# Kernel tuning notes

Hardware: AMD Instinct MI355X
Metric: run time of the kernel (lower is better)

## Reference

```python
import jax, jax.numpy as jnp
import numpy as np

N_NODES = 100000
N_EDGES = 1600000
N_GRAPHS = 1024
DIM_IN = 128
DIM_SELF = 16
BN_EPS = 1e-5


def _bn(x, gamma, beta):
    # training-mode BatchNorm1d over dim 0 (biased variance, as torch uses for normalization)
    m = jnp.mean(x, axis=0)
    v = jnp.mean((x - m) ** 2, axis=0)
    return gamma * (x - m) * jax.lax.rsqrt(v + BN_EPS) + beta


def _mlp(x, W1, b1, g, b, W2, b2):
    h = x @ W1 + b1
    h = jax.nn.relu(_bn(h, g, b))
    return h @ W2 + b2


def _gin(h, src, dst, W1, b1, g, b, W2, b2):
    # GINConv with eps=0: (1+eps)*h + sum over in-neighbors, then MLP
    agg = jax.ops.segment_sum(h[src], dst, num_segments=N_NODES)
    return _mlp(h + agg, W1, b1, g, b, W2, b2)


def setup_inputs() -> dict:
    key = jax.random.key(0)
    ks = jax.random.split(key, 16)

    def lin(k, fan_in, fan_out):
        bound = 1.0 / np.sqrt(fan_in)
        k1, k2 = jax.random.split(k)
        W = jax.random.uniform(k1, (fan_in, fan_out), jnp.float32, -bound, bound)
        b = jax.random.uniform(k2, (fan_out,), jnp.float32, -bound, bound)
        return W, b

    inp = {}
    inp['feat'] = jax.random.normal(ks[0], (N_NODES, DIM_IN), jnp.float32)
    inp['self_feat'] = jax.random.normal(ks[1], (N_GRAPHS, DIM_SELF), jnp.float32)
    inp['edge_src'] = jax.random.randint(ks[2], (N_EDGES,), 0, N_NODES, jnp.int32)
    inp['edge_dst'] = jax.random.randint(ks[3], (N_EDGES,), 0, N_NODES, jnp.int32)
    inp['node2graph'] = jnp.sort(jax.random.randint(ks[4], (N_NODES,), 0, N_GRAPHS, jnp.int32))

    inp['g1_W1'], inp['g1_b1'] = lin(ks[5], DIM_IN, 100)
    inp['g1_gamma'] = jnp.ones((100,), jnp.float32)
    inp['g1_beta'] = jnp.zeros((100,), jnp.float32)
    inp['g1_W2'], inp['g1_b2'] = lin(ks[6], 100, 100)

    inp['g2_W1'], inp['g2_b1'] = lin(ks[7], 100, 20)
    inp['g2_gamma'] = jnp.ones((20,), jnp.float32)
    inp['g2_beta'] = jnp.zeros((20,), jnp.float32)
    inp['g2_W2'], inp['g2_b2'] = lin(ks[8], 20, 20)

    inp['fc1_W'], inp['fc1_b'] = lin(ks[9], 20 * DIM_SELF, 32)
    inp['bn1_gamma'] = jnp.ones((32,), jnp.float32)
    inp['bn1_beta'] = jnp.zeros((32,), jnp.float32)
    inp['fc2_W'], inp['fc2_b'] = lin(ks[10], 32, 8)
    inp['bn2_gamma'] = jnp.ones((8,), jnp.float32)
    inp['bn2_beta'] = jnp.zeros((8,), jnp.float32)
    inp['fc3_W'], inp['fc3_b'] = lin(ks[11], 8, 1)
    return inp


def reference(feat, self_feat,
              g1_W1, g1_b1, g1_gamma, g1_beta, g1_W2, g1_b2,
              g2_W1, g2_b1, g2_gamma, g2_beta, g2_W2, g2_b2,
              fc1_W, fc1_b, bn1_gamma, bn1_beta,
              fc2_W, fc2_b, bn2_gamma, bn2_beta,
              fc3_W, fc3_b,
              edge_src, edge_dst, node2graph):
    h = _gin(feat, edge_src, edge_dst, g1_W1, g1_b1, g1_gamma, g1_beta, g1_W2, g1_b2)
    h = jax.nn.relu(h)
    h = _gin(h, edge_src, edge_dst, g2_W1, g2_b1, g2_gamma, g2_beta, g2_W2, g2_b2)
    h = jax.nn.relu(h)  # [N, 20]

    # dgl.mean_nodes: per-graph mean of node features
    sums = jax.ops.segment_sum(h, node2graph, num_segments=N_GRAPHS)  # [B, 20]
    cnts = jax.ops.segment_sum(jnp.ones((N_NODES,), h.dtype), node2graph, num_segments=N_GRAPHS)
    hg = sums / jnp.maximum(cnts, 1.0)[:, None]

    # kronecker fusion: bmm([B,20,1],[B,1,dim_self]) -> flatten
    kron = jnp.einsum('bi,bj->bij', hg, self_feat).reshape(N_GRAPHS, -1)  # [B, 20*dim_self]

    out = jax.nn.relu(_bn(kron @ fc1_W + fc1_b, bn1_gamma, bn1_beta))
    # dropout(0.3) is identity in eval mode
    out = jax.nn.relu(_bn(out @ fc2_W + fc2_b, bn2_gamma, bn2_beta))
    out = out @ fc3_W + fc3_b  # [B, dim_out]
    return out
```

## Files before the change

### kernel.cpp

```cpp
#include <hip/hip_runtime.h>

#define NN 100000
#define NE 1600000
#define NG 1024
#define DIN 128
#define D1 100
#define D2 20
#define DSELF 16
#define BN_EPS 1e-5f

#define NB 391
#define NBLK 782
#define EPB 2048
#define RAWCAP 5120
#define NAGG2 4000
#define NREP 64
#define APITCH 136

typedef unsigned int uint;
typedef unsigned short ushort;
typedef __attribute__((ext_vector_type(8))) short bfv8;
typedef __attribute__((ext_vector_type(4))) float fv4;

__device__ inline float bflo(uint x) { return __uint_as_float(x << 16); }
__device__ inline float bfhi(uint x) { return __uint_as_float(x & 0xffff0000u); }
__device__ inline uint packbf2(float a, float b) {
    uint ua = __float_as_uint(a), ub = __float_as_uint(b);
    ua += 0x7fffu + ((ua >> 16) & 1u);
    ub += 0x7fffu + ((ub >> 16) & 1u);
    return (ua >> 16) | (ub & 0xffff0000u);
}
__device__ inline ushort bfr(float x) {
    uint u = __float_as_uint(x);
    u += 0x7fffu + ((u >> 16) & 1u);
    return (ushort)(u >> 16);
}

__global__ __launch_bounds__(256) void k_gemm1(const float* __restrict__ feat,
                                               const float* __restrict__ W1,
                                               ushort* __restrict__ z1bf,
                                               float* __restrict__ pb1r) {
    __shared__ __align__(16) char smem[64 * APITCH * 2 + 112 * APITCH * 2];
    ushort* Al = (ushort*)smem;
    ushort* Bt = (ushort*)(smem + 64 * APITCH * 2);
    int t = threadIdx.x;
    if (blockIdx.x == 0) {
        for (int i = t; i < NREP * 200; i += 256) pb1r[i] = 0.f;
    }
    int row0 = blockIdx.x * 64;
#pragma unroll
    for (int i = 0; i < 8; i++) {
        int p = i * 256 + t;
        int r = p >> 5, cq = p & 31;
        int row = row0 + r; if (row >= NN) row = NN - 1;
        float4 v = *(const float4*)(feat + (size_t)row * DIN + cq * 4);
        ushort* dst = Al + r * APITCH + 4 * cq;
        dst[0] = bfr(v.x); dst[1] = bfr(v.y); dst[2] = bfr(v.z); dst[3] = bfr(v.w);
    }
    for (int p = t; p < 12800; p += 256) {
        int k = p / 100, n = p % 100;
        Bt[n * APITCH + k] = bfr(W1[p]);
    }
    __syncthreads();
    int w = __builtin_amdgcn_readfirstlane(t >> 6);
    int l = t & 63;
    int m16 = l & 15, quad = l >> 4;
    fv4 acc[7];
#pragma unroll
    for (int nt = 0; nt < 7; nt++) acc[nt] = (fv4){0.f, 0.f, 0.f, 0.f};
    const ushort* arow = Al + (w * 16 + m16) * APITCH;
#pragma unroll
    for (int kk = 0; kk < 4; kk++) {
        int kb = kk * 32 + quad * 8;
        bfv8 a = *(const bfv8*)(arow + kb);
#pragma unroll
        for (int nt = 0; nt < 7; nt++) {
            bfv8 b = *(const bfv8*)(Bt + (nt * 16 + m16) * APITCH + kb);
            acc[nt] = __builtin_amdgcn_mfma_f32_16x16x32_bf16(a, b, acc[nt], 0, 0, 0);
        }
    }
    __syncthreads();
    float* Ep = (float*)smem;
#pragma unroll
    for (int nt = 0; nt < 7; nt++) {
        int n = nt * 16 + m16;
        if (n < 100) {
#pragma unroll
            for (int rix = 0; rix < 4; rix++)
                Ep[(w * 16 + quad * 4 + rix) * 101 + n] = acc[nt][rix];
        }
    }
    __syncthreads();
#pragma unroll
    for (int i = 0; i < 13; i++) {
        int p = i * 256 + t;
        if (p < 3200) {
            int rr = p / 50, cc = 2 * (p % 50);
            int row = row0 + rr;
            if (row < NN) {
                float v0 = Ep[rr * 101 + cc], v1 = Ep[rr * 101 + cc + 1];
                *(uint*)(z1bf + (size_t)row * 100 + cc) = packbf2(v0, v1);
            }
        }
    }
}

__global__ __launch_bounds__(256) void k_csrA1(const int* __restrict__ dst,
                                               int* __restrict__ pbcount) {
    __shared__ int h[NB];
    int t = threadIdx.x, blk = blockIdx.x;
    for (int i = t; i < NB; i += 256) h[i] = 0;
    __syncthreads();
    int e0 = blk * EPB + t;
#pragma unroll
    for (int i = 0; i < 8; i++) {
        int e = e0 + i * 256;
        if (e < NE) atomicAdd(&h[dst[e] >> 8], 1);
    }
    __syncthreads();
    for (int i = t; i < NB; i += 256) pbcount[i * NBLK + blk] = h[i];
}

__global__ __launch_bounds__(1024) void k_csrS1(int* __restrict__ pbcount,
                                                int* __restrict__ btot) {
    __shared__ int s[1024];
    int t = threadIdx.x, b = blockIdx.x;
    int v = (t < NBLK) ? pbcount[b * NBLK + t] : 0;
    s[t] = v;
    __syncthreads();
    for (int off = 1; off < 1024; off <<= 1) {
        int x = (t >= off) ? s[t - off] : 0;
        __syncthreads();
        s[t] += x;
        __syncthreads();
    }
    if (t < NBLK) pbcount[b * NBLK + t] = s[t] - v;
    if (t == 1023) btot[b] = s[t];
}

__global__ __launch_bounds__(256) void k_csrA2(const int* __restrict__ src,
                                               const int* __restrict__ dst,
                                               const int* __restrict__ pbexcl,
                                               const int* __restrict__ btot,
                                               int* __restrict__ ebase_g,
                                               uint* __restrict__ gbuf) {
    __shared__ int cur[NB];
    __shared__ int sa[512], sb[512];
    int t = threadIdx.x, blk = blockIdx.x;
    int o0 = (t < NB) ? btot[t] : 0;
    int o1 = (t + 256 < NB) ? btot[t + 256] : 0;
    sa[t] = o0; sa[t + 256] = o1;
    __syncthreads();
    int* sp = sa; int* dp = sb;
    for (int off = 1; off < 512; off <<= 1) {
        dp[t] = sp[t] + ((t >= off) ? sp[t - off] : 0);
        int i2 = t + 256;
        dp[i2] = sp[i2] + ((i2 >= off) ? sp[i2 - off] : 0);
        __syncthreads();
        int* tmp = sp; sp = dp; dp = tmp;
    }
    if (t < NB)       cur[t]       = (sp[t] - o0) + pbexcl[t * NBLK + blk];
    if (t + 256 < NB) cur[t + 256] = (sp[t + 256] - o1) + pbexcl[(t + 256) * NBLK + blk];
    if (blk == 0) {
        if (t < NB)       ebase_g[t]       = sp[t] - o0;
        if (t + 256 < NB) ebase_g[t + 256] = sp[t + 256] - o1;
        if (t == 0)       ebase_g[NB]      = sp[NB - 1];
    }
    __syncthreads();
    int e0 = blk * EPB + t;
#pragma unroll
    for (int i = 0; i < 8; i++) {
        int e = e0 + i * 256;
        if (e < NE) {
            int d = dst[e];
            int b = d >> 8;
            int pos = atomicAdd(&cur[b], 1);
            gbuf[pos] = (uint)src[e] | ((uint)(d & 255) << 17);
        }
    }
}

__global__ __launch_bounds__(256) void k_csrB(const uint* __restrict__ gbuf,
                                              const int* __restrict__ ebase,
                                              int* __restrict__ deg,
                                              int* __restrict__ offs,
                                              int* __restrict__ srcS) {
    __shared__ uint raw[RAWCAP];
    __shared__ int srt[RAWCAP];
    __shared__ int pref[256], cur[256];
    int t = threadIdx.x, b = blockIdx.x;
    int e0 = ebase[b], e1 = ebase[b + 1];
    int cnt = e1 - e0; if (cnt > RAWCAP) cnt = RAWCAP;
    cur[t] = 0;
    for (int i = t; i < cnt; i += 256) raw[i] = gbuf[e0 + i];
    __syncthreads();
    for (int i = t; i < cnt; i += 256) atomicAdd(&cur[raw[i] >> 17], 1);
    __syncthreads();
    int v = cur[t];
    pref[t] = v;
    __syncthreads();
    for (int off = 1; off < 256; off <<= 1) {
        int x = (t >= off) ? pref[t - off] : 0;
        __syncthreads();
        pref[t] += x;
        __syncthreads();
    }
    int excl = pref[t] - v;
    int node = b * 256 + t;
    if (node < NN) { deg[node] = v; offs[node] = e0 + excl; }
    cur[t] = excl;
    __syncthreads();
    for (int i = t; i < cnt; i += 256) {
        uint p = raw[i];
        int lpos = atomicAdd(&cur[p >> 17], 1);
        srt[lpos] = (int)(p & 0x1FFFFu);
    }
    __syncthreads();
    for (int i = t; i < cnt; i += 256) srcS[e0 + i] = srt[i];
}

__global__ __launch_bounds__(1024) void k_agg1(const ushort* __restrict__ z1bf,
                                               const int* __restrict__ offs,
                                               const int* __restrict__ deg,
                                               const int* __restrict__ srcS,
                                               ushort* __restrict__ u1b,
                                               float* __restrict__ pb1r) {
    __shared__ float part[16][200];
    int t = threadIdx.x;
    int wq = __builtin_amdgcn_readfirstlane(t >> 6);
    int l = t & 63;
    int n = blockIdx.x * 16 + wq;
    int d = 0, base = 0;
    if (n < NN) { d = deg[n]; base = offs[n]; }
    bool act = (l < 50) && (n < NN);
    const ushort* zc = z1bf + 2 * l;
    float a0 = 0.f, a1 = 0.f, b0 = 0.f, b1 = 0.f;
    float c0 = 0.f, c1 = 0.f, e0 = 0.f, e1 = 0.f;
    int i = 0;
    for (; i + 8 <= d; i += 8) {
        int s0 = srcS[base + i],     s1 = srcS[base + i + 1];
        int s2 = srcS[base + i + 2], s3 = srcS[base + i + 3];
        int s4 = srcS[base + i + 4], s5 = srcS[base + i + 5];
        int s6 = srcS[base + i + 6], s7 = srcS[base + i + 7];
        if (act) {
            uint x0 = *(const uint*)(zc + (size_t)s0 * 100);
            uint x1 = *(const uint*)(zc + (size_t)s1 * 100);
            uint x2 = *(const uint*)(zc + (size_t)s2 * 100);
            uint x3 = *(const uint*)(zc + (size_t)s3 * 100);
            uint x4 = *(const uint*)(zc + (size_t)s4 * 100);
            uint x5 = *(const uint*)(zc + (size_t)s5 * 100);
            uint x6 = *(const uint*)(zc + (size_t)s6 * 100);
            uint x7 = *(const uint*)(zc + (size_t)s7 * 100);
            a0 += bflo(x0); a1 += bfhi(x0);
            b0 += bflo(x1); b1 += bfhi(x1);
            c0 += bflo(x2); c1 += bfhi(x2);
            e0 += bflo(x3); e1 += bfhi(x3);
            a0 += bflo(x4); a1 += bfhi(x4);
            b0 += bflo(x5); b1 += bfhi(x5);
            c0 += bflo(x6); c1 += bfhi(x6);
            e0 += bflo(x7); e1 += bfhi(x7);
        }
    }
    for (; i + 2 <= d; i += 2) {
        int s0 = srcS[base + i], s1 = srcS[base + i + 1];
        if (act) {
            uint x0 = *(const uint*)(zc + (size_t)s0 * 100);
            uint x1 = *(const uint*)(zc + (size_t)s1 * 100);
            a0 += bflo(x0); a1 += bfhi(x0);
            b0 += bflo(x1); b1 += bfhi(x1);
        }
    }
    if (i < d) {
        int s0 = srcS[base + i];
        if (act) {
            uint x0 = *(const uint*)(zc + (size_t)s0 * 100);
            a0 += bflo(x0); a1 += bfhi(x0);
        }
    }
    float r0 = 0.f, r1 = 0.f;
    if (act) {
        uint xs = *(const uint*)(zc + (size_t)n * 100);
        r0 = (a0 + b0) + (c0 + e0) + bflo(xs);
        r1 = (a1 + b1) + (c1 + e1) + bfhi(xs);
        *(uint*)(u1b + (size_t)n * 100 + 2 * l) = packbf2(r0, r1);
    }
    if (l < 50) {
        part[wq][2 * l] = r0;            part[wq][2 * l + 1] = r1;
        part[wq][100 + 2 * l] = r0 * r0; part[wq][100 + 2 * l + 1] = r1 * r1;
    }
    __syncthreads();
    if (t < 200) {
        float s = 0.f;
#pragma unroll
        for (int w2 = 0; w2 < 16; w2++) s += part[w2][t];
        atomicAdd(&pb1r[(blockIdx.x & (NREP - 1)) * 200 + t], s);
    }
}

__global__ __launch_bounds__(256) void k_bnfin100(const float* __restrict__ pb1r,
                                                  const float* __restrict__ gamma,
                                                  const float* __restrict__ beta,
                                                  float* __restrict__ sc,
                                                  float* __restrict__ sh) {
    __shared__ float red[200];
    int t = threadIdx.x;
    if (t < 200) {
        float s = 0.f;
#pragma unroll 8
        for (int r = 0; r < NREP; r++) s += pb1r[r * 200 + t];
        red[t] = s;
    }
    __syncthreads();
    if (t < 100) {
        float S = red[t], Q = red[100 + t];
        float mean = S * (1.f / NN);
        float var = Q * (1.f / NN) - mean * mean;
        float inv = rsqrtf(var + BN_EPS);
        float s = gamma[t] * inv;
        sc[t] = s;
        sh[t] = beta[t] - mean * s;
    }
}

__global__ __launch_bounds__(256) void k_m2(const ushort* __restrict__ u1b,
                                            const float* __restrict__ sc,
                                            const float* __restrict__ sh,
                                            const float* __restrict__ W2,
                                            const float* __restrict__ b2,
                                            const float* __restrict__ W1p,
                                            ushort* __restrict__ z2bf,
                                            float* __restrict__ pb2r) {
    __shared__ float Xs[100 * 65];
    int t = threadIdx.x;
    if (blockIdx.x == 0) {
        for (int i = t; i < NREP * 40; i += 256) pb2r[i] = 0.f;
    }
    int row0 = blockIdx.x * 64;
#pragma unroll
    for (int i = 0; i < 13; i++) {
        int p = i * 256 + t;
        if (p < 3200) {
            int r = p / 50, c = 2 * (p % 50);
            int row = row0 + r; if (row >= NN) row = NN - 1;
            uint x = *(const uint*)(u1b + (size_t)row * 100 + c);
            Xs[c * 65 + r] = fmaxf(bflo(x) * sc[c] + sh[c], 0.f);
            Xs[(c + 1) * 65 + r] = fmaxf(bfhi(x) * sc[c + 1] + sh[c + 1], 0.f);
        }
    }
    __syncthreads();
    int cg = __builtin_amdgcn_readfirstlane(t >> 6);
    int r = t & 63;
    int j0 = cg * 25;
    float H[25];
#pragma unroll
    for (int m = 0; m < 25; m++) H[m] = 0.f;
    for (int k = 0; k < D1; k++) {
        float a = Xs[k * 65 + r];
        const float* wr = W2 + k * D1 + j0;
#pragma unroll
        for (int m = 0; m < 25; m++) H[m] = fmaf(a, wr[m], H[m]);
    }
#pragma unroll
    for (int m = 0; m < 25; m++) H[m] = fmaxf(H[m] + b2[j0 + m], 0.f);
    float pz[20];
#pragma unroll
    for (int c = 0; c < 20; c++) pz[c] = 0.f;
#pragma unroll
    for (int m = 0; m < 25; m++) {
        const float* wp = W1p + (j0 + m) * D2;
#pragma unroll
        for (int c = 0; c < 20; c++) pz[c] = fmaf(H[m], wp[c], pz[c]);
    }
    __syncthreads();
    float* red = Xs;
#pragma unroll
    for (int c = 0; c < 20; c++) red[t * 20 + c] = pz[c];
    __syncthreads();
#pragma unroll
    for (int i = 0; i < 3; i++) {
        int p = i * 256 + t;
        if (p < 640) {
            int rr = p / 10, c2 = 2 * (p % 10);
            int row = row0 + rr;
            if (row < NN) {
                float v0 = red[rr * 20 + c2] + red[(64 + rr) * 20 + c2] +
                           red[(128 + rr) * 20 + c2] + red[(192 + rr) * 20 + c2];
                float v1 = red[rr * 20 + c2 + 1] + red[(64 + rr) * 20 + c2 + 1] +
                           red[(128 + rr) * 20 + c2 + 1] + red[(192 + rr) * 20 + c2 + 1];
                *(uint*)(z2bf + (size_t)row * 32 + c2) = packbf2(v0, v1);
            }
        }
    }
}

__global__ __launch_bounds__(256) void k_agg2(const ushort* __restrict__ z2bf,
                                              const int* __restrict__ offs,
                                              const int* __restrict__ deg,
                                              const int* __restrict__ srcS,
                                              float* __restrict__ u2,
                                              float* __restrict__ pb2r) {
    __shared__ float ls[500], lq[500];
    int t = threadIdx.x;
    int n = blockIdx.x * 25 + t / 10;
    int c2 = 2 * (t % 10);
    float r0 = 0.f, r1 = 0.f;
    if (t < 250 && n < NN) {
        int d = deg[n], base = offs[n];
        const ushort* zc = z2bf + c2;
        float a0 = 0.f, a1 = 0.f, b0 = 0.f, b1 = 0.f;
        int i = 0;
        for (; i + 2 <= d; i += 2) {
            uint x0 = *(const uint*)(zc + (size_t)srcS[base + i] * 32);
            uint x1 = *(const uint*)(zc + (size_t)srcS[base + i + 1] * 32);
            a0 += bflo(x0); a1 += bfhi(x0);
            b0 += bflo(x1); b1 += bfhi(x1);
        }
        if (i < d) {
            uint x0 = *(const uint*)(zc + (size_t)srcS[base + i] * 32);
            a0 += bflo(x0); a1 += bfhi(x0);
        }
        uint xs = *(const uint*)(zc + (size_t)n * 32);
        r0 = a0 + b0 + bflo(xs);
        r1 = a1 + b1 + bfhi(xs);
        *(float2*)(u2 + (size_t)n * D2 + c2) = make_float2(r0, r1);
    }
    if (t < 250) {
        int idx = (t / 10) * 20 + c2;
        ls[idx] = r0;     lq[idx] = r0 * r0;
        ls[idx + 1] = r1; lq[idx + 1] = r1 * r1;
    }
    __syncthreads();
    if (t < 20) {
        float S = 0.f, Q = 0.f;
#pragma unroll
        for (int j = 0; j < 25; j++) { S += ls[j * 20 + t]; Q += lq[j * 20 + t]; }
        int rep = (blockIdx.x & (NREP - 1)) * 40;
        atomicAdd(&pb2r[rep + t], S);
        atomicAdd(&pb2r[rep + 20 + t], Q);
    }
}

__global__ __launch_bounds__(64) void k_bnfin20(const float* __restrict__ pb2r,
                                                const float* __restrict__ gamma,
                                                const float* __restrict__ beta,
                                                float* __restrict__ sc,
                                                float* __restrict__ sh) {
    __shared__ float red[40];
    int t = threadIdx.x;
    if (t < 40) {
        float s = 0.f;
#pragma unroll 8
        for (int r = 0; r < NREP; r++) s += pb2r[r * 40 + t];
        red[t] = s;
    }
    __syncthreads();
    if (t < 20) {
        float S = red[t], Q = red[20 + t];
        float mean = S * (1.f / NN);
        float var = Q * (1.f / NN) - mean * mean;
        float inv = rsqrtf(var + BN_EPS);
        float s = gamma[t] * inv;
        sc[t] = s;
        sh[t] = beta[t] - mean * s;
    }
}

__global__ __launch_bounds__(256) void k_m3(const float* __restrict__ u2,
                                            const float* __restrict__ sc,
                                            const float* __restrict__ sh,
                                            const float* __restrict__ W2p,
                                            const float* __restrict__ b2p,
                                            float* __restrict__ h2) {
    int row = blockIdx.x * 256 + threadIdx.x;
    if (row >= NN) return;
    float ya[20];
    const float4* up = (const float4*)(u2 + (size_t)row * D2);
#pragma unroll
    for (int i = 0; i < 5; i++) {
        float4 v = up[i];
        float4 S = *(const float4*)(sc + 4 * i);
        float4 H = *(const float4*)(sh + 4 * i);
        ya[4 * i + 0] = fmaxf(v.x * S.x + H.x, 0.f);
        ya[4 * i + 1] = fmaxf(v.y * S.y + H.y, 0.f);
        ya[4 * i + 2] = fmaxf(v.z * S.z + H.z, 0.f);
        ya[4 * i + 3] = fmaxf(v.w * S.w + H.w, 0.f);
    }
    float hrow[D2];
#pragma unroll
    for (int j = 0; j < D2; j++) {
        float h = b2p[j];
#pragma unroll
        for (int k = 0; k < D2; k++) h = fmaf(ya[k], W2p[k * D2 + j], h);
        hrow[j] = fmaxf(h, 0.f);
    }
    float* hr = h2 + (size_t)row * D2;
#pragma unroll
    for (int c = 0; c < D2; c += 4) {
        float4 o; o.x = hrow[c]; o.y = hrow[c + 1]; o.z = hrow[c + 2]; o.w = hrow[c + 3];
        *(float4*)(hr + c) = o;
    }
}

__global__ __launch_bounds__(256) void k_pool(const float* __restrict__ h2,
                                              const int* __restrict__ n2g,
                                              float* __restrict__ hg) {
    int wq = __builtin_amdgcn_readfirstlane(threadIdx.x >> 6);
    int l = threadIdx.x & 63;
    int g = blockIdx.x * 4 + wq;
    if (g >= NG) return;
    int lo = 0, hi = NN;
    while (lo < hi) { int mid = (lo + hi) >> 1; if (n2g[mid] < g) lo = mid + 1; else hi = mid; }
    int s0 = lo;
    hi = NN;
    while (lo < hi) { int mid = (lo + hi) >> 1; if (n2g[mid] < g + 1) lo = mid + 1; else hi = mid; }
    int s1 = lo;
    float a = 0.f;
    if (l < 60) {
        int rg = l / 20, c = l % 20;
        for (int n = s0 + rg; n < s1; n += 3) a += h2[(size_t)n * D2 + c];
    }
    float v1 = __shfl(a, l + 20, 64);
    float v2 = __shfl(a, l + 40, 64);
    if (l < 20) {
        float cnt = (float)(s1 - s0);
        hg[g * D2 + l] = (a + v1 + v2) / fmaxf(cnt, 1.f);
    }
}

__global__ void k_head1(const float* __restrict__ hg, const float* __restrict__ sf,
                        const float* __restrict__ fc1W, float* __restrict__ a1) {
    int b = blockIdx.x * 8 + threadIdx.x / 32;
    int c = threadIdx.x % 32;
    if (b >= NG) return;
    const float* hgb = hg + b * D2;
    const float* sfb = sf + b * DSELF;
    float acc = 0.f;
    for (int i = 0; i < D2; i++) {
        float hi = hgb[i];
#pragma unroll
        for (int j = 0; j < DSELF; j++)
            acc += hi * sfb[j] * fc1W[(i * DSELF + j) * 32 + c];
    }
    a1[b * 32 + c] = acc;
}

__global__ __launch_bounds__(1024) void k_head2(
    const float* __restrict__ a1, const float* __restrict__ g1,
    const float* __restrict__ be1, const float* __restrict__ fc2W,
    const float* __restrict__ g2, const float* __restrict__ be2,
    const float* __restrict__ fc3W, const float* __restrict__ fc3b,
    float* __restrict__ out) {
    int t = threadIdx.x;
    int lane = t & 63, w = t >> 6;
    __shared__ float s1[16][32], s2[16][32];
    __shared__ float sc[32], sh[32], sc2[8], sh2[8];
    float x[32];
    const float4* ap = (const float4*)(a1 + t * 32);
#pragma unroll
    for (int i = 0; i < 8; i++) {
        float4 v = ap[i];
        x[4 * i] = v.x; x[4 * i + 1] = v.y; x[4 * i + 2] = v.z; x[4 * i + 3] = v.w;
    }
#pragma unroll
    for (int c = 0; c < 32; c++) {
        float v = x[c], q = v * v;
        for (int o = 32; o > 0; o >>= 1) {
            v += __shfl_down(v, o, 64);
            q += __shfl_down(q, o, 64);
        }
        if (lane == 0) { s1[w][c] = v; s2[w][c] = q; }
    }
    __syncthreads();
    if (t < 32) {
        float s = 0.f, q = 0.f;
        for (int ww = 0; ww < 16; ww++) { s += s1[ww][t]; q += s2[ww][t]; }
        float mean = s * (1.f / NG);
        float var = q * (1.f / NG) - mean * mean;
        float inv = rsqrtf(var + BN_EPS);
        float scl = g1[t] * inv;
        sc[t] = scl;
        sh[t] = be1[t] - mean * scl;
    }
    __syncthreads();
#pragma unroll
    for (int c = 0; c < 32; c++) x[c] = fmaxf(x[c] * sc[c] + sh[c], 0.f);
    float y[8];
#pragma unroll
    for (int p = 0; p < 8; p++) {
        float a = 0.f;
#pragma unroll
        for (int c = 0; c < 32; c++) a += x[c] * fc2W[c * 8 + p];
        y[p] = a;
    }
    __syncthreads();
#pragma unroll
    for (int p = 0; p < 8; p++) {
        float v = y[p], q = v * v;
        for (int o = 32; o > 0; o >>= 1) {
            v += __shfl_down(v, o, 64);
            q += __shfl_down(q, o, 64);
        }
        if (lane == 0) { s1[w][p] = v; s2[w][p] = q; }
    }
    __syncthreads();
    if (t < 8) {
        float s = 0.f, q = 0.f;
        for (int ww = 0; ww < 16; ww++) { s += s1[ww][t]; q += s2[ww][t]; }
        float mean = s * (1.f / NG);
        float var = q * (1.f / NG) - mean * mean;
        float inv = rsqrtf(var + BN_EPS);
        float scl = g2[t] * inv;
        sc2[t] = scl;
        sh2[t] = be2[t] - mean * scl;
    }
    __syncthreads();
    float o = fc3b[0];
#pragma unroll
    for (int p = 0; p < 8; p++) {
        float yy = fmaxf(y[p] * sc2[p] + sh2[p], 0.f);
        o += yy * fc3W[p];
    }
    out[t] = o;
}

extern "C" void kernel_launch(void* const* d_in, const int* in_sizes, int n_in,
                              void* d_out, int out_size, void* d_ws, size_t ws_size,
                              hipStream_t stream) {
    const float* feat    = (const float*)d_in[0];
    const float* sf      = (const float*)d_in[1];
    const int*   esrc    = (const int*)d_in[2];
    const int*   edst    = (const int*)d_in[3];
    const int*   n2g     = (const int*)d_in[4];
    const float* g1W1    = (const float*)d_in[5];
    const float* g1gam   = (const float*)d_in[7];
    const float* g1bet   = (const float*)d_in[8];
    const float* g1W2    = (const float*)d_in[9];
    const float* g1b2    = (const float*)d_in[10];
    const float* g2W1    = (const float*)d_in[11];
    const float* g2gam   = (const float*)d_in[13];
    const float* g2bet   = (const float*)d_in[14];
    const float* g2W2    = (const float*)d_in[15];
    const float* g2b2    = (const float*)d_in[16];
    const float* fc1W    = (const float*)d_in[17];
    const float* hbn1g   = (const float*)d_in[19];
    const float* hbn1b   = (const float*)d_in[20];
    const float* fc2W    = (const float*)d_in[21];
    const float* hbn2g   = (const float*)d_in[23];
    const float* hbn2b   = (const float*)d_in[24];
    const float* fc3W    = (const float*)d_in[25];
    const float* fc3b    = (const float*)d_in[26];
    float* out = (float*)d_out;

    char* w = (char*)d_ws;
    size_t off = 0;
    auto alloc = [&](size_t bytes) -> char* {
        char* p = w + off;
        off += (bytes + 15) & ~(size_t)15;
        return p;
    };
    char* regA = alloc((size_t)NN * 128 * 2);
    ushort* z1bf = (ushort*)regA;
    ushort* z2bf = (ushort*)regA;
    float*  u2   = (float*)(regA + 6400000);
    float*  h2   = (float*)(regA + 14400000);
    ushort* u1b  = (ushort*)alloc((size_t)NN * 100 * 2);
    int*   pbcnt = (int*)alloc((size_t)NB * NBLK * 4);
    int*   btot  = (int*)alloc(NB * 4);
    int*   ebase = (int*)alloc((NB + 1) * 4);
    uint*  gbuf  = (uint*)alloc((size_t)NE * 4);
    int*   deg   = (int*)alloc(NN * 4);
    int*   offs  = (int*)alloc(NN * 4);
    int*   srcS  = (int*)alloc((size_t)NE * 4);
    float* pb1r  = (float*)alloc((size_t)NREP * 200 * 4);
    float* pb2r  = (float*)alloc((size_t)NREP * 40 * 4);
    float* sc1   = (float*)alloc(D1 * 4);
    float* sh1   = (float*)alloc(D1 * 4);
    float* sc2   = (float*)alloc(D2 * 4);
    float* sh2   = (float*)alloc(D2 * 4);
    float* hg    = (float*)alloc(NG * D2 * 4);
    float* a1    = (float*)alloc(NG * 32 * 4);
    (void)in_sizes; (void)n_in; (void)out_size; (void)ws_size;

    k_gemm1<<<(NN + 63) / 64, 256, 0, stream>>>(feat, g1W1, z1bf, pb1r);

    k_csrA1<<<NBLK, 256, 0, stream>>>(edst, pbcnt);
    k_csrS1<<<NB, 1024, 0, stream>>>(pbcnt, btot);
    k_csrA2<<<NBLK, 256, 0, stream>>>(esrc, edst, pbcnt, btot, ebase, gbuf);
    k_csrB<<<NB, 256, 0, stream>>>(gbuf, ebase, deg, offs, srcS);

    k_agg1<<<NN / 16, 1024, 0, stream>>>(z1bf, offs, deg, srcS, u1b, pb1r);
    k_bnfin100<<<1, 256, 0, stream>>>(pb1r, g1gam, g1bet, sc1, sh1);
    k_m2<<<(NN + 63) / 64, 256, 0, stream>>>(u1b, sc1, sh1, g1W2, g1b2, g2W1, z2bf, pb2r);

    k_agg2<<<NAGG2, 256, 0, stream>>>(z2bf, offs, deg, srcS, u2, pb2r);
    k_bnfin20<<<1, 64, 0, stream>>>(pb2r, g2gam, g2bet, sc2, sh2);
    k_m3<<<(NN + 255) / 256, 256, 0, stream>>>(u2, sc2, sh2, g2W2, g2b2, h2);

    k_pool<<<(NG + 3) / 4, 256, 0, stream>>>(h2, n2g, hg);
    k_head1<<<NG / 8, 256, 0, stream>>>(hg, sf, fc1W, a1);
    k_head2<<<1, 1024, 0, stream>>>(a1, hbn1g, hbn1b, fc2W, hbn2g, hbn2b, fc3W, fc3b, out);
}
```

Baseline: 429.6 us.

## Pad z1 rows to 128 and process 16 nodes per wave in agg1

Pads the bf16 z1 gather buffer to a 128-element row pitch so that each gathered row starts on a 256-byte boundary. The agg1 kernel now uses 256-thread blocks where each wave walks 16 consecutive nodes. Each wave keeps its BatchNorm sum and sum-of-squares in registers and issues per-lane atomics once at the end, which removes the shared-memory reduction and the block-wide barrier. The cost is a larger z1 buffer and longer serial work per wave, which can leave waves unevenly loaded when node degrees differ.

```diff
diff --git a/kernel.cpp b/kernel.cpp
--- a/kernel.cpp
+++ b/kernel.cpp
@@ -99,7 +99,7 @@
             int row = row0 + rr;
             if (row < NN) {
                 float v0 = Ep[rr * 101 + cc], v1 = Ep[rr * 101 + cc + 1];
-                *(uint*)(z1bf + (size_t)row * 100 + cc) = packbf2(v0, v1);
+                *(uint*)(z1bf + (size_t)row * 128 + cc) = packbf2(v0, v1);
             }
         }
     }
@@ -219,81 +219,81 @@
     for (int i = t; i < cnt; i += 256) srcS[e0 + i] = srt[i];
 }
 
-__global__ __launch_bounds__(1024) void k_agg1(const ushort* __restrict__ z1bf,
-                                               const int* __restrict__ offs,
-                                               const int* __restrict__ deg,
-                                               const int* __restrict__ srcS,
-                                               ushort* __restrict__ u1b,
-                                               float* __restrict__ pb1r) {
-    __shared__ float part[16][200];
-    int t = threadIdx.x;
-    int wq = __builtin_amdgcn_readfirstlane(t >> 6);
-    int l = t & 63;
-    int n = blockIdx.x * 16 + wq;
-    int d = 0, base = 0;
-    if (n < NN) { d = deg[n]; base = offs[n]; }
-    bool act = (l < 50) && (n < NN);
+__global__ __launch_bounds__(256) void k_agg1(const ushort* __restrict__ z1bf,
+                                              const int* __restrict__ offs,
+                                              const int* __restrict__ deg,
+                                              const int* __restrict__ srcS,
+                                              ushort* __restrict__ u1b,
+                                              float* __restrict__ pb1r) {
+    int wv = __builtin_amdgcn_readfirstlane(threadIdx.x >> 6);
+    int wid = blockIdx.x * 4 + wv;
+    int l = threadIdx.x & 63;
+    bool act = l < 50;
     const ushort* zc = z1bf + 2 * l;
-    float a0 = 0.f, a1 = 0.f, b0 = 0.f, b1 = 0.f;
-    float c0 = 0.f, c1 = 0.f, e0 = 0.f, e1 = 0.f;
-    int i = 0;
-    for (; i + 8 <= d; i += 8) {
-        int s0 = srcS[base + i],     s1 = srcS[base + i + 1];
-        int s2 = srcS[base + i + 2], s3 = srcS[base + i + 3];
-        int s4 = srcS[base + i + 4], s5 = srcS[base + i + 5];
-        int s6 = srcS[base + i + 6], s7 = srcS[base + i + 7];
+    float S0 = 0.f, S1 = 0.f, Q0 = 0.f, Q1 = 0.f;
+    int n0 = wid * 16;
+    for (int k = 0; k < 16; k++) {
+        int n = n0 + k;
+        if (n >= NN) break;
+        int d = deg[n], base = offs[n];
+        float a0 = 0.f, a1 = 0.f, b0 = 0.f, b1 = 0.f;
+        float c0 = 0.f, c1 = 0.f, e0 = 0.f, e1 = 0.f;
+        int i = 0;
+        for (; i + 8 <= d; i += 8) {
+            int s0 = srcS[base + i],     s1 = srcS[base + i + 1];
+            int s2 = srcS[base + i + 2], s3 = srcS[base + i + 3];
+            int s4 = srcS[base + i + 4], s5 = srcS[base + i + 5];
+            int s6 = srcS[base + i + 6], s7 = srcS[base + i + 7];
+            if (act) {
+                uint x0 = *(const uint*)(zc + (size_t)s0 * 128);
+                uint x1 = *(const uint*)(zc + (size_t)s1 * 128);
+                uint x2 = *(const uint*)(zc + (size_t)s2 * 128);
+                uint x3 = *(const uint*)(zc + (size_t)s3 * 128);
+                uint x4 = *(const uint*)(zc + (size_t)s4 * 128);
+                uint x5 = *(const uint*)(zc + (size_t)s5 * 128);
+                uint x6 = *(const uint*)(zc + (size_t)s6 * 128);
+                uint x7 = *(const uint*)(zc + (size_t)s7 * 128);
+                a0 += bflo(x0); a1 += bfhi(x0);
+                b0 += bflo(x1); b1 += bfhi(x1);
+                c0 += bflo(x2); c1 += bfhi(x2);
+                e0 += bflo(x3); e1 += bfhi(x3);
+                a0 += bflo(x4); a1 += bfhi(x4);
+                b0 += bflo(x5); b1 += bfhi(x5);
+                c0 += bflo(x6); c1 += bfhi(x6);
+                e0 += bflo(x7); e1 += bfhi(x7);
+            }
+        }
+        for (; i + 2 <= d; i += 2) {
+            int s0 = srcS[base + i], s1 = srcS[base + i + 1];
+            if (act) {
+                uint x0 = *(const uint*)(zc + (size_t)s0 * 128);
+                uint x1 = *(const uint*)(zc + (size_t)s1 * 128);
+                a0 += bflo(x0); a1 += bfhi(x0);
+                b0 += bflo(x1); b1 += bfhi(x1);
+            }
+        }
+        if (i < d) {
+            int s0 = srcS[base + i];
+            if (act) {
+                uint x0 = *(const uint*)(zc + (size_t)s0 * 128);
+                a0 += bflo(x0); a1 += bfhi(x0);
+            }
+        }
         if (act) {
-            uint x0 = *(const uint*)(zc + (size_t)s0 * 100);
-            uint x1 = *(const uint*)(zc + (size_t)s1 * 100);
-            uint x2 = *(const uint*)(zc + (size_t)s2 * 100);
-            uint x3 = *(const uint*)(zc + (size_t)s3 * 100);
-            uint x4 = *(const uint*)(zc + (size_t)s4 * 100);
-            uint x5 = *(const uint*)(zc + (size_t)s5 * 100);
-            uint x6 = *(const uint*)(zc + (size_t)s6 * 100);
-            uint x7 = *(const uint*)(zc + (size_t)s7 * 100);
-            a0 += bflo(x0); a1 += bfhi(x0);
-            b0 += bflo(x1); b1 += bfhi(x1);
-            c0 += bflo(x2); c1 += bfhi(x2);
-            e0 += bflo(x3); e1 += bfhi(x3);
-            a0 += bflo(x4); a1 += bfhi(x4);
-            b0 += bflo(x5); b1 += bfhi(x5);
-            c0 += bflo(x6); c1 += bfhi(x6);
-            e0 += bflo(x7); e1 += bfhi(x7);
-        }
-    }
-    for (; i + 2 <= d; i += 2) {
-        int s0 = srcS[base + i], s1 = srcS[base + i + 1];
-        if (act) {
-            uint x0 = *(const uint*)(zc + (size_t)s0 * 100);
-            uint x1 = *(const uint*)(zc + (size_t)s1 * 100);
-            a0 += bflo(x0); a1 += bfhi(x0);
-            b0 += bflo(x1); b1 += bfhi(x1);
-        }
-    }
-    if (i < d) {
-        int s0 = srcS[base + i];
-        if (act) {
-            uint x0 = *(const uint*)(zc + (size_t)s0 * 100);
-            a0 += bflo(x0); a1 += bfhi(x0);
-        }
-    }
-    float r0 = 0.f, r1 = 0.f;
+            uint xs = *(const uint*)(zc + (size_t)n * 128);
+            float r0 = (a0 + b0) + (c0 + e0) + bflo(xs);
+            float r1 = (a1 + b1) + (c1 + e1) + bfhi(xs);
+            *(uint*)(u1b + (size_t)n * 100 + 2 * l) = packbf2(r0, r1);
+            S0 += r0; S1 += r1;
+            Q0 = fmaf(r0, r0, Q0); Q1 = fmaf(r1, r1, Q1);
+        }
+    }
     if (act) {
-        uint xs = *(const uint*)(zc + (size_t)n * 100);
-        r0 = (a0 + b0) + (c0 + e0) + bflo(xs);
-        r1 = (a1 + b1) + (c1 + e1) + bfhi(xs);
-        *(uint*)(u1b + (size_t)n * 100 + 2 * l) = packbf2(r0, r1);
-    }
-    if (l < 50) {
-        part[wq][2 * l] = r0;            part[wq][2 * l + 1] = r1;
-        part[wq][100 + 2 * l] = r0 * r0; part[wq][100 + 2 * l + 1] = r1 * r1;
-    }
-    __syncthreads();
-    if (t < 200) {
-        float s = 0.f;
-#pragma unroll
-        for (int w2 = 0; w2 < 16; w2++) s += part[w2][t];
-        atomicAdd(&pb1r[(blockIdx.x & (NREP - 1)) * 200 + t], s);
+        float* rep = pb1r + (wid & (NREP - 1)) * 200;
+        atomicAdd(&rep[2 * l], S0);
+        atomicAdd(&rep[2 * l + 1], S1);
+        atomicAdd(&rep[100 + 2 * l], Q0);
+        atomicAdd(&rep[100 + 2 * l + 1], Q1);
     }
 }
 
@@ -688,7 +688,7 @@
     k_csrA2<<<NBLK, 256, 0, stream>>>(esrc, edst, pbcnt, btot, ebase, gbuf);
     k_csrB<<<NB, 256, 0, stream>>>(gbuf, ebase, deg, offs, srcS);
 
-    k_agg1<<<NN / 16, 1024, 0, stream>>>(z1bf, offs, deg, srcS, u1b, pb1r);
+    k_agg1<<<1563, 256, 0, stream>>>(z1bf, offs, deg, srcS, u1b, pb1r);
     k_bnfin100<<<1, 256, 0, stream>>>(pb1r, g1gam, g1bet, sc1, sh1);
     k_m2<<<(NN + 63) / 64, 256, 0, stream>>>(u1b, sc1, sh1, g1W2, g1b2, g2W1, z2bf, pb2r);
 
```

Result: slower. 439.9 us (+2.4%).
